# Performance work log

Measured on AMD Instinct MI355X. Metric: run time of the kernel, lower is better.

Reference implementation:

```python
import jax, jax.numpy as jnp
import numpy as np

D_IN = 1024
D_OUT = 1024
NUM_HEADS = 16
HEAD_DIM = D_OUT // NUM_HEADS


def setup_inputs() -> dict:
    key = jax.random.key(0)
    ks = jax.random.split(key, 6)
    s = 0.02
    return {
        "x": jax.random.normal(ks[0], (4, 2048, D_IN), dtype=jnp.float32),
        "W_q": jax.random.normal(ks[1], (D_IN, D_OUT), dtype=jnp.float32) * s,
        "W_k": jax.random.normal(ks[2], (D_IN, D_OUT), dtype=jnp.float32) * s,
        "W_v": jax.random.normal(ks[3], (D_IN, D_OUT), dtype=jnp.float32) * s,
        "W_o": jax.random.normal(ks[4], (D_OUT, D_OUT), dtype=jnp.float32) * s,
        "b_o": jax.random.normal(ks[5], (D_OUT,), dtype=jnp.float32) * s,
    }


def reference(x, W_q, W_k, W_v, W_o, b_o):
    b, n, _ = x.shape
    # project and split heads: [b, h, n, d]
    q = (x @ W_q).reshape(b, n, NUM_HEADS, HEAD_DIM).transpose(0, 2, 1, 3)
    k = (x @ W_k).reshape(b, n, NUM_HEADS, HEAD_DIM).transpose(0, 2, 1, 3)
    v = (x @ W_v).reshape(b, n, NUM_HEADS, HEAD_DIM).transpose(0, 2, 1, 3)
    scores = jnp.einsum("bhqd,bhkd->bhqk", q, k)
    causal = jnp.tril(jnp.ones((n, n), dtype=bool))  # True = keep
    scores = jnp.where(causal, scores, -jnp.inf)
    attn = jax.nn.softmax(scores / np.sqrt(HEAD_DIM).astype(np.float32), axis=-1)
    ctx = jnp.einsum("bhqk,bhkd->bhqd", attn, v)
    ctx = ctx.transpose(0, 2, 1, 3).reshape(b, n, D_OUT)
    return ctx @ W_o + b_o
```

## Files before the change

kernel.cpp:

```cpp
#include <hip/hip_runtime.h>
#include <hip/hip_bf16.h>

#define NHEADS 16
#define HDIM 64
#define SEQ 2048
#define BATCH 4
#define DMODEL 1024
#define MTOT (BATCH * SEQ)

typedef short v8s __attribute__((ext_vector_type(8)));
typedef short v4s __attribute__((ext_vector_type(4)));
typedef float v4f __attribute__((ext_vector_type(4)));
typedef float v16f __attribute__((ext_vector_type(16)));
typedef unsigned int v4u __attribute__((ext_vector_type(4)));
typedef unsigned short u16;
typedef unsigned int u32;

__device__ __forceinline__ u16 f2bf(float f) {
    union { float f; unsigned u; } v; v.f = f;
    unsigned r = v.u + 0x7FFFu + ((v.u >> 16) & 1u);
    return (u16)(r >> 16);
}

__device__ __forceinline__ void g2l16(const u16* g, short* l) {
    __builtin_amdgcn_global_load_lds(
        (const __attribute__((address_space(1))) u32*)g,
        (__attribute__((address_space(3))) u32*)l, 16, 0, 0);
}

__device__ __forceinline__ unsigned pk_bf16(float a, float b) {
    unsigned r;
    asm("v_cvt_pk_bf16_f32 %0, %1, %2" : "=v"(r) : "v"(a), "v"(b));
    return r;
}
__device__ __forceinline__ void pl32swap(unsigned& x, unsigned& y) {
    asm("v_permlane32_swap_b32 %0, %1" : "+v"(x), "+v"(y));
}
__device__ __forceinline__ v8s build_pa(float a0, float a1, float a2, float a3,
                                        float b0, float b1, float b2, float b3) {
    unsigned X  = pk_bf16(a0, a1);
    unsigned X2 = pk_bf16(a2, a3);
    unsigned Y  = pk_bf16(b0, b1);
    unsigned Y2 = pk_bf16(b2, b3);
    pl32swap(X, Y);
    pl32swap(X2, Y2);
    v4u w; w[0] = X; w[1] = X2; w[2] = Y; w[3] = Y2;
    return __builtin_bit_cast(v8s, w);
}

__global__ __launch_bounds__(256)
void xcvt(const float* __restrict__ x, u16* __restrict__ xb)
{
    size_t i = ((size_t)blockIdx.x * 256 + threadIdx.x) * 8;
    v4f a = *(const v4f*)&x[i];
    v4f b = *(const v4f*)&x[i + 4];
    v8s p;
#pragma unroll
    for (int e = 0; e < 4; ++e) p[e] = (short)f2bf(a[e]);
#pragma unroll
    for (int e = 0; e < 4; ++e) p[4 + e] = (short)f2bf(b[e]);
    *(v8s*)&xb[i] = p;
}

__device__ __forceinline__ void transpose_body(
    const float* __restrict__ src, u16* __restrict__ dst, int k0, int n0)
{
    __shared__ __align__(8) short Ts[64 * 68];
    const int t = threadIdx.x;
    const int n4 = (t & 15) * 4, kl = t >> 4;
#pragma unroll
    for (int it = 0; it < 4; ++it) {
        int k = kl + 16 * it;
        v4f v = *(const v4f*)&src[(size_t)(k0 + k) * DMODEL + n0 + n4];
        v4s p;
#pragma unroll
        for (int e = 0; e < 4; ++e) p[e] = (short)f2bf(v[e]);
        *(v4s*)&Ts[k * 68 + n4] = p;
    }
    __syncthreads();
    const int nl = t >> 4, k4 = (t & 15) * 4;
#pragma unroll
    for (int it = 0; it < 4; ++it) {
        int n = nl + 16 * it;
        v4s o;
#pragma unroll
        for (int e = 0; e < 4; ++e) o[e] = Ts[(k4 + e) * 68 + n];
        *(v4s*)&dst[(size_t)(n0 + n) * DMODEL + k0 + k4] = o;
    }
}

__global__ __launch_bounds__(256)
void transpose_w(const float* __restrict__ src, u16* __restrict__ dst)
{
    transpose_body(src, dst, blockIdx.x * 64, blockIdx.y * 64);
}

__global__ __launch_bounds__(256)
void transpose_w4(const float* __restrict__ s0, const float* __restrict__ s1,
                  const float* __restrict__ s2, const float* __restrict__ s3,
                  u16* __restrict__ dst)
{
    const int z = blockIdx.z;
    const float* src = (z == 0) ? s0 : (z == 1) ? s1 : (z == 2) ? s2 : s3;
    transpose_body(src, dst + (size_t)z * DMODEL * DMODEL,
                   blockIdx.x * 64, blockIdx.y * 64);
}

#define QSCALE (0.125f * 1.44269504088896f)

__device__ __forceinline__ void qkv_epilogue(
    v4f (&acc)[4][4], int which, int n0, int m0, int wn, int wm,
    int l15, int quad, u16* Qb, u16* Kb, u16* Vt)
{
    if (which == 2) {
#pragma unroll
        for (int i = 0; i < 4; ++i)
#pragma unroll
            for (int j = 0; j < 4; ++j) {
                int col = n0 + wn + j * 16 + l15;
                int h = col >> 6, d = col & 63;
                int m = m0 + wm + i * 16 + quad * 4;
                int b = m >> 11, n = m & (SEQ - 1);
                v4s pv;
#pragma unroll
                for (int r = 0; r < 4; ++r) pv[r] = (short)f2bf(acc[i][j][r]);
                *(v4s*)&Vt[((size_t)(b * NHEADS + h) * HDIM + d) * SEQ + n] = pv;
            }
    } else {
        u16* Ob = (which == 0) ? Qb : Kb;
        const float scale = (which == 0) ? QSCALE : 1.0f;
#pragma unroll
        for (int i = 0; i < 4; ++i)
#pragma unroll
            for (int j = 0; j < 4; ++j) {
                int col = n0 + wn + j * 16 + l15;
                int h = col >> 6, d = col & 63;
#pragma unroll
                for (int r = 0; r < 4; ++r) {
                    int m = m0 + wm + i * 16 + quad * 4 + r;
                    int b = m >> 11, n = m & (SEQ - 1);
                    Ob[((size_t)(b * NHEADS + h) * SEQ + n) * HDIM + d] =
                        f2bf(acc[i][j][r] * scale);
                }
            }
    }
}

__global__ __launch_bounds__(256, 2)
void qkv_fast(const u16* __restrict__ xb, const u16* __restrict__ Wt,
              u16* __restrict__ Qb, u16* __restrict__ Kb, u16* __restrict__ Vt)
{
    __shared__ __align__(16) short As[128 * 64];
    __shared__ __align__(16) short Bs[128 * 64];

    const int which = blockIdx.z;
    const u16* W = Wt + (size_t)which * DMODEL * DMODEL;

    const int n0 = blockIdx.x * 128;
    const int m0 = blockIdx.y * 128;
    const int t = threadIdx.x;
    const int lane = t & 63;
    const int l15 = lane & 15;
    const int quad = lane >> 4;
    const int wave = t >> 6;
    const int wm = (wave >> 1) * 64;
    const int wn = (wave & 1) * 64;
    const int srow = t >> 3;
    const int sc8 = (t & 7) * 8;

    v4f acc[4][4];
#pragma unroll
    for (int i = 0; i < 4; ++i)
#pragma unroll
        for (int j = 0; j < 4; ++j) acc[i][j] = {0.f, 0.f, 0.f, 0.f};

    for (int k0 = 0; k0 < DMODEL; k0 += 64) {
        __syncthreads();
#pragma unroll
        for (int c = 0; c < 4; ++c) {
            g2l16(&xb[(size_t)(m0 + c * 32 + srow) * DMODEL + k0 + sc8],
                  &As[(c * 32 + srow) * 64 + sc8]);
            g2l16(&W[(size_t)(n0 + c * 32 + srow) * DMODEL + k0 + sc8],
                  &Bs[(c * 32 + srow) * 64 + sc8]);
        }
        __syncthreads();

#pragma unroll
        for (int kh = 0; kh < 2; ++kh) {
            v8s af[4], bf[4];
#pragma unroll
            for (int i = 0; i < 4; ++i)
                af[i] = *(const v8s*)
                    &As[(wm + i * 16 + l15) * 64 + kh * 32 + quad * 8];
#pragma unroll
            for (int j = 0; j < 4; ++j)
                bf[j] = *(const v8s*)
                    &Bs[(wn + j * 16 + l15) * 64 + kh * 32 + quad * 8];
#pragma unroll
            for (int i = 0; i < 4; ++i)
#pragma unroll
                for (int j = 0; j < 4; ++j)
                    acc[i][j] = __builtin_amdgcn_mfma_f32_16x16x32_bf16(
                        af[i], bf[j], acc[i][j], 0, 0, 0);
        }
    }
    qkv_epilogue(acc, which, n0, m0, wn, wm, l15, quad, Qb, Kb, Vt);
}

__global__ __launch_bounds__(256, 2)
void qkv_slow(const float* __restrict__ x, const u16* __restrict__ Wt,
              u16* __restrict__ Qb, u16* __restrict__ Kb, u16* __restrict__ Vt)
{
    __shared__ __align__(16) short As[128 * 32];
    __shared__ __align__(16) short Bs[128 * 32];

    const int which = blockIdx.z;
    const u16* W = Wt + (size_t)which * DMODEL * DMODEL;

    const int n0 = blockIdx.x * 128;
    const int m0 = blockIdx.y * 128;
    const int t = threadIdx.x;
    const int lane = t & 63;
    const int l15 = lane & 15;
    const int quad = lane >> 4;
    const int wave = t >> 6;
    const int wm = (wave >> 1) * 64;
    const int wn = (wave & 1) * 64;
    const int srow = t >> 2;
    const int sc8 = (t & 3) * 8;

    v4f acc[4][4];
#pragma unroll
    for (int i = 0; i < 4; ++i)
#pragma unroll
        for (int j = 0; j < 4; ++j) acc[i][j] = {0.f, 0.f, 0.f, 0.f};

    for (int k0 = 0; k0 < DMODEL; k0 += 32) {
        __syncthreads();
        g2l16(&W[(size_t)(n0 + srow) * DMODEL + k0 + sc8], &Bs[srow * 32 + sc8]);
        g2l16(&W[(size_t)(n0 + 64 + srow) * DMODEL + k0 + sc8],
              &Bs[(64 + srow) * 32 + sc8]);
#pragma unroll
        for (int it = 0; it < 2; ++it) {
            int row = srow + 64 * it;
            const float* xp = &x[(size_t)(m0 + row) * DMODEL + k0 + sc8];
            v4f x0 = *(const v4f*)xp;
            v4f x1 = *(const v4f*)(xp + 4);
            v8s av;
#pragma unroll
            for (int e = 0; e < 4; ++e) av[e] = (short)f2bf(x0[e]);
#pragma unroll
            for (int e = 0; e < 4; ++e) av[4 + e] = (short)f2bf(x1[e]);
            *(v8s*)&As[row * 32 + sc8] = av;
        }
        __syncthreads();

        v8s af[4], bf[4];
#pragma unroll
        for (int i = 0; i < 4; ++i)
            af[i] = *(const v8s*)&As[(wm + i * 16 + l15) * 32 + quad * 8];
#pragma unroll
        for (int j = 0; j < 4; ++j)
            bf[j] = *(const v8s*)&Bs[(wn + j * 16 + l15) * 32 + quad * 8];
#pragma unroll
        for (int i = 0; i < 4; ++i)
#pragma unroll
            for (int j = 0; j < 4; ++j)
                acc[i][j] = __builtin_amdgcn_mfma_f32_16x16x32_bf16(
                    af[i], bf[j], acc[i][j], 0, 0, 0);
    }
    qkv_epilogue(acc, which, n0, m0, wn, wm, l15, quad, Qb, Kb, Vt);
}

#define KP 72

__global__ __launch_bounds__(256, 2)
void attn(const u16* __restrict__ Qb, const u16* __restrict__ Kb,
          const u16* __restrict__ Vt, u16* __restrict__ Cx)
{
    __shared__ __align__(16) short Ks[64 * KP];
    __shared__ __align__(16) short Vs[64 * KP];

    const int ell = blockIdx.x;
    const int xcd = ell & 7;
    const int rest = ell >> 3;
    const int p = rest & 7;
    const int bh = ((rest >> 3) << 3) | xcd;

    const int t = threadIdx.x;
    const int lane = t & 63;
    const int l31 = lane & 31;
    const int hi = lane >> 5;
    const int wave = t >> 6;
    const int koff = hi * 8;

    const u16* Qh = Qb + (size_t)bh * SEQ * HDIM;
    const u16* Kh = Kb + (size_t)bh * SEQ * HDIM;
    const u16* Vh = Vt + (size_t)bh * HDIM * SEQ;

    const int skey = t >> 2;
    const int sd = (t & 3) * 16;
    const int b = bh >> 4, h = bh & 15;

#pragma unroll 1
    for (int phase = 0; phase < 2; ++phase) {
        const int qt = phase ? p : (15 - p);
        const int q0w = qt * 128 + wave * 32;
        const int kmax = 2 * qt + 1;

        v8s qf[4];
#pragma unroll
        for (int dc = 0; dc < 4; ++dc)
            qf[dc] = *(const v8s*)
                &Qh[(size_t)(q0w + l31) * HDIM + dc * 16 + koff];

        v16f o0, o1;
#pragma unroll
        for (int r = 0; r < 16; ++r) { o0[r] = 0.f; o1[r] = 0.f; }
        float ls = 0.f;

        v8s pk0_, pk1_, pv0_, pv1_;
        {
            const u16* Kp = &Kh[(size_t)skey * HDIM + sd];
            pk0_ = *(const v8s*)Kp; pk1_ = *(const v8s*)(Kp + 8);
            const u16* Vp = &Vh[(size_t)skey * SEQ + sd];
            pv0_ = *(const v8s*)Vp; pv1_ = *(const v8s*)(Vp + 8);
        }

#pragma unroll 1
        for (int kb = 0; kb <= kmax; ++kb) {
            __syncthreads();
            *(v8s*)&Ks[skey * KP + sd] = pk0_;
            *(v8s*)&Ks[skey * KP + sd + 8] = pk1_;
            *(v8s*)&Vs[skey * KP + sd] = pv0_;
            *(v8s*)&Vs[skey * KP + sd + 8] = pv1_;
            __syncthreads();

            if (kb < kmax) {
                const u16* Kp = &Kh[(size_t)((kb + 1) * 64 + skey) * HDIM + sd];
                pk0_ = *(const v8s*)Kp; pk1_ = *(const v8s*)(Kp + 8);
                const u16* Vp = &Vh[(size_t)skey * SEQ + (kb + 1) * 64 + sd];
                pv0_ = *(const v8s*)Vp; pv1_ = *(const v8s*)(Vp + 8);
            }

            if (kb * 64 <= q0w + 31) {
                const bool diag = (kb * 64 + 63 > q0w);
                const int qrow = q0w + l31;

                v16f st0, st1;
#pragma unroll
                for (int r = 0; r < 16; ++r) { st0[r] = 0.f; st1[r] = 0.f; }
#pragma unroll
                for (int dc = 0; dc < 4; ++dc) {
                    v8s kf0 = *(const v8s*)&Ks[l31 * KP + dc * 16 + koff];
                    v8s kf1 = *(const v8s*)
                        &Ks[(32 + l31) * KP + dc * 16 + koff];
                    st0 = __builtin_amdgcn_mfma_f32_32x32x16_bf16(
                        kf0, qf[dc], st0, 0, 0, 0);
                    st1 = __builtin_amdgcn_mfma_f32_32x32x16_bf16(
                        kf1, qf[dc], st1, 0, 0, 0);
                }

                v16f pe0, pe1;
                if (!diag) {
#pragma unroll
                    for (int r = 0; r < 16; ++r) {
                        pe0[r] = exp2f(st0[r]);
                        pe1[r] = exp2f(st1[r]);
                    }
                } else {
#pragma unroll
                    for (int r = 0; r < 16; ++r) {
                        int kl = kb * 64 + (r & 3) + 8 * (r >> 2) + 4 * hi;
                        pe0[r] = (kl > qrow) ? 0.f : exp2f(st0[r]);
                        pe1[r] = (kl + 32 > qrow) ? 0.f : exp2f(st1[r]);
                    }
                }
#pragma unroll
                for (int r = 0; r < 16; ++r) ls += pe0[r] + pe1[r];

                v8s pa0 = build_pa(pe0[0], pe0[1], pe0[2], pe0[3],
                                   pe0[4], pe0[5], pe0[6], pe0[7]);
                v8s pa1 = build_pa(pe0[8], pe0[9], pe0[10], pe0[11],
                                   pe0[12], pe0[13], pe0[14], pe0[15]);
                v8s pa2 = build_pa(pe1[0], pe1[1], pe1[2], pe1[3],
                                   pe1[4], pe1[5], pe1[6], pe1[7]);
                v8s pa3 = build_pa(pe1[8], pe1[9], pe1[10], pe1[11],
                                   pe1[12], pe1[13], pe1[14], pe1[15]);

#pragma unroll
                for (int kc = 0; kc < 4; ++kc) {
                    v8s pav = (kc == 0) ? pa0 : (kc == 1) ? pa1
                              : (kc == 2) ? pa2 : pa3;
                    v8s vf0 = *(const v8s*)&Vs[l31 * KP + kc * 16 + koff];
                    v8s vf1 = *(const v8s*)
                        &Vs[(32 + l31) * KP + kc * 16 + koff];
                    o0 = __builtin_amdgcn_mfma_f32_32x32x16_bf16(
                        pav, vf0, o0, 0, 0, 0);
                    o1 = __builtin_amdgcn_mfma_f32_32x32x16_bf16(
                        pav, vf1, o1, 0, 0, 0);
                }
            }
        }

        ls += __shfl_xor(ls, 32, 64);
        float inv = 1.f / ls;
#pragma unroll
        for (int r = 0; r < 16; ++r) {
            int m = (r & 3) + 8 * (r >> 2) + 4 * hi;
            float im = __shfl(inv, m, 64);
            size_t idx = ((size_t)(b * SEQ + q0w + m)) * DMODEL
                         + h * HDIM + l31;
            Cx[idx] = f2bf(o0[r] * im);
            Cx[idx + 32] = f2bf(o1[r] * im);
        }
    }
}

__global__ __launch_bounds__(256, 2)
void out_gemm(const u16* __restrict__ Cx, const u16* __restrict__ WoT,
              const float* __restrict__ bo, float* __restrict__ Y)
{
    __shared__ __align__(16) short As[128 * 64];
    __shared__ __align__(16) short Bs[128 * 64];

    const int n0 = blockIdx.x * 128;
    const int m0 = blockIdx.y * 128;
    const int t = threadIdx.x;
    const int lane = t & 63;
    const int l15 = lane & 15;
    const int quad = lane >> 4;
    const int wave = t >> 6;
    const int wm = (wave >> 1) * 64;
    const int wn = (wave & 1) * 64;
    const int srow = t >> 3;
    const int sc8 = (t & 7) * 8;

    v4f acc[4][4];
#pragma unroll
    for (int i = 0; i < 4; ++i)
#pragma unroll
        for (int j = 0; j < 4; ++j) acc[i][j] = {0.f, 0.f, 0.f, 0.f};

    for (int k0 = 0; k0 < DMODEL; k0 += 64) {
        __syncthreads();
#pragma unroll
        for (int c = 0; c < 4; ++c) {
            g2l16(&Cx[(size_t)(m0 + c * 32 + srow) * DMODEL + k0 + sc8],
                  &As[(c * 32 + srow) * 64 + sc8]);
            g2l16(&WoT[(size_t)(n0 + c * 32 + srow) * DMODEL + k0 + sc8],
                  &Bs[(c * 32 + srow) * 64 + sc8]);
        }
        __syncthreads();

#pragma unroll
        for (int kh = 0; kh < 2; ++kh) {
            v8s af[4], bf[4];
#pragma unroll
            for (int i = 0; i < 4; ++i)
                af[i] = *(const v8s*)
                    &As[(wm + i * 16 + l15) * 64 + kh * 32 + quad * 8];
#pragma unroll
            for (int j = 0; j < 4; ++j)
                bf[j] = *(const v8s*)
                    &Bs[(wn + j * 16 + l15) * 64 + kh * 32 + quad * 8];
#pragma unroll
            for (int i = 0; i < 4; ++i)
#pragma unroll
                for (int j = 0; j < 4; ++j)
                    acc[i][j] = __builtin_amdgcn_mfma_f32_16x16x32_bf16(
                        af[i], bf[j], acc[i][j], 0, 0, 0);
        }
    }

#pragma unroll
    for (int i = 0; i < 4; ++i)
#pragma unroll
        for (int j = 0; j < 4; ++j) {
            int col = n0 + wn + j * 16 + l15;
            float bias = bo[col];
#pragma unroll
            for (int r = 0; r < 4; ++r) {
                int m = m0 + wm + i * 16 + quad * 4 + r;
                Y[(size_t)m * DMODEL + col] = acc[i][j][r] + bias;
            }
        }
}

extern "C" void kernel_launch(void* const* d_in, const int* in_sizes, int n_in,
                              void* d_out, int out_size, void* d_ws,
                              size_t ws_size, hipStream_t stream)
{
    const float* x  = (const float*)d_in[0];
    const float* Wq = (const float*)d_in[1];
    const float* Wk = (const float*)d_in[2];
    const float* Wv = (const float*)d_in[3];
    const float* Wo = (const float*)d_in[4];
    const float* bo = (const float*)d_in[5];
    float* Y = (float*)d_out;

    const size_t per = (size_t)BATCH * NHEADS * SEQ * HDIM;
    const size_t wsz = (size_t)DMODEL * DMODEL;
    u16* base = (u16*)d_ws;

    if (ws_size >= (size_t)72 * 1024 * 1024) {
        u16* xb  = base;
        u16* Cx  = base;
        u16* Wt4 = base + per;
        u16* Qb  = base + per + 4 * wsz;
        u16* Kb  = Qb + per;
        u16* Vt  = Kb + per;

        xcvt<<<MTOT * DMODEL / (256 * 8), 256, 0, stream>>>(x, xb);
        transpose_w4<<<dim3(16, 16, 4), 256, 0, stream>>>(Wq, Wk, Wv, Wo, Wt4);
        qkv_fast<<<dim3(DMODEL / 128, MTOT / 128, 3), 256, 0, stream>>>(
            xb, Wt4, Qb, Kb, Vt);
        attn<<<512, 256, 0, stream>>>(Qb, Kb, Vt, Cx);
        out_gemm<<<dim3(DMODEL / 128, MTOT / 128), 256, 0, stream>>>(
            Cx, Wt4 + 3 * wsz, bo, Y);
    } else {
        u16* Wt  = base;
        u16* Cx  = base;
        u16* Qb  = base + per;
        u16* WoT = base + per;
        u16* Kb  = base + 2 * per;
        u16* Vt  = base + 3 * per;

        transpose_w<<<dim3(16, 16), 256, 0, stream>>>(Wq, Wt);
        transpose_w<<<dim3(16, 16), 256, 0, stream>>>(Wk, Wt + wsz);
        transpose_w<<<dim3(16, 16), 256, 0, stream>>>(Wv, Wt + 2 * wsz);
        qkv_slow<<<dim3(DMODEL / 128, MTOT / 128, 3), 256, 0, stream>>>(
            x, Wt, Qb, Kb, Vt);
        attn<<<512, 256, 0, stream>>>(Qb, Kb, Vt, Cx);
        transpose_w<<<dim3(16, 16), 256, 0, stream>>>(Wo, WoT);
        out_gemm<<<dim3(DMODEL / 128, MTOT / 128), 256, 0, stream>>>(
            Cx, WoT, bo, Y);
    }
}
```

Before: 266.5 us.

## Replace QKV GEMM with 256x256 double-buffered pipelined kernel over fused QKV

Swaps the 128x128 single-buffered QKV projection kernel for a 512-thread kernel with 256x256 tiles that treats the three weight matrices as one concatenated N=3072 operand. The new kernel double-buffers LDS, overlaps global-to-LDS staging with MFMA work across four sub-phases, applies an XOR swizzle to LDS to avoid bank conflicts, raises wave priority around MFMA blocks, and remaps block ids for better L2 locality. The aim is more operand reuse and better load/compute overlap in the GEMM. In exchange it uses much more LDS (128 KB) and registers, which limits occupancy, and it depends on hand-tuned waitcnt/barrier ordering.

```diff
diff --git a/kernel.cpp b/kernel.cpp
--- a/kernel.cpp
+++ b/kernel.cpp
@@ -108,6 +108,162 @@
 
 #define QSCALE (0.125f * 1.44269504088896f)
 
+#define BAR() __builtin_amdgcn_s_barrier()
+#define LGKM0() do { asm volatile("s_waitcnt lgkmcnt(0)" ::: "memory"); \
+                     __builtin_amdgcn_sched_barrier(0); } while (0)
+
+#define STAGE_A(sbuf, stile, half, issue) \
+    g2l16(&xb[(size_t)(m0 + (half) * 128 + (issue) * 64 + srr) * DMODEL + \
+              (stile) * 64 + scol], \
+          &As[sbuf][(half) * 8192 + (issue) * 4096 + t * 8])
+#define STAGE_B(sbuf, stile, half, issue) \
+    g2l16(&Wt[(size_t)(n0g + (half) * 128 + (issue) * 64 + srr) * DMODEL + \
+              (stile) * 64 + scol], \
+          &Bs[sbuf][(half) * 8192 + (issue) * 4096 + t * 8])
+
+#define LDA_QUAD(bb, I0) \
+    _Pragma("unroll") \
+    for (int i = 0; i < 4; ++i) \
+        _Pragma("unroll") \
+        for (int kh = 0; kh < 2; ++kh) \
+            af[i][kh] = *(const v8s*)&As[bb][ \
+                (wm * 128 + ((I0) + i) * 16 + l15) * 64 + \
+                (((kh * 4 + quad) ^ (l15 & 7)) << 3)];
+
+#define LDB_PAIR(bb, J0) \
+    _Pragma("unroll") \
+    for (int j = 0; j < 2; ++j) \
+        _Pragma("unroll") \
+        for (int kh = 0; kh < 2; ++kh) \
+            bf[(J0) + j][kh] = *(const v8s*)&Bs[bb][ \
+                (wn * 64 + ((J0) + j) * 16 + l15) * 64 + \
+                (((kh * 4 + quad) ^ (l15 & 7)) << 3)];
+
+#define MFMA_QUAD(I0, J0) \
+    _Pragma("unroll") \
+    for (int i = 0; i < 4; ++i) \
+        _Pragma("unroll") \
+        for (int j = 0; j < 2; ++j) \
+            _Pragma("unroll") \
+            for (int kh = 0; kh < 2; ++kh) \
+                acc[(I0) + i][(J0) + j] = \
+                    __builtin_amdgcn_mfma_f32_16x16x32_bf16( \
+                        af[i][kh], bf[(J0) + j][kh], \
+                        acc[(I0) + i][(J0) + j], 0, 0, 0);
+
+__global__ __launch_bounds__(512, 2)
+void qkv256(const u16* __restrict__ xb, const u16* __restrict__ Wt,
+            u16* __restrict__ Qb, u16* __restrict__ Kb, u16* __restrict__ Vt)
+{
+    __shared__ __align__(16) short As[2][256 * 64];
+    __shared__ __align__(16) short Bs[2][256 * 64];
+
+    const int bid = blockIdx.x;
+    const int swz = (bid & 7) * 48 + (bid >> 3);
+    const int bx = swz % 12, by = swz / 12;
+    const int n0g = bx * 256;
+    const int m0 = by * 256;
+
+    const int t = threadIdx.x;
+    const int lane = t & 63;
+    const int l15 = lane & 15;
+    const int quad = lane >> 4;
+    const int wave = t >> 6;
+    const int wm = wave >> 2;
+    const int wn = wave & 3;
+
+    const int srr = t >> 3;
+    const int scol = (((t & 7) ^ (srr & 7)) << 3);
+
+    v4f acc[8][4];
+#pragma unroll
+    for (int i = 0; i < 8; ++i)
+#pragma unroll
+        for (int j = 0; j < 4; ++j) acc[i][j] = {0.f, 0.f, 0.f, 0.f};
+
+    STAGE_A(0, 0, 0, 0); STAGE_A(0, 0, 0, 1);
+    STAGE_A(0, 0, 1, 0); STAGE_A(0, 0, 1, 1);
+    STAGE_B(0, 0, 0, 0); STAGE_B(0, 0, 0, 1);
+    STAGE_B(0, 0, 1, 0); STAGE_B(0, 0, 1, 1);
+    STAGE_B(1, 1, 0, 0); STAGE_B(1, 1, 0, 1);
+    STAGE_B(1, 1, 1, 0); STAGE_B(1, 1, 1, 1);
+    asm volatile("s_waitcnt vmcnt(4)" ::: "memory");
+    BAR();
+
+#pragma unroll 1
+    for (int tt = 0; tt < 16; ++tt) {
+        const int cb = tt & 1;
+        v8s af[4][2];
+        v8s bf[4][2];
+
+        LDA_QUAD(cb, 0);
+        LDB_PAIR(cb, 0);
+        if (tt < 15) { STAGE_A(cb ^ 1, tt + 1, 0, 0);
+                       STAGE_A(cb ^ 1, tt + 1, 0, 1); }
+        BAR();
+        LGKM0();
+        __builtin_amdgcn_s_setprio(1);
+        MFMA_QUAD(0, 0);
+        __builtin_amdgcn_s_setprio(0);
+        BAR();
+
+        LDB_PAIR(cb, 2);
+        if (tt < 15) { STAGE_A(cb ^ 1, tt + 1, 1, 0);
+                       STAGE_A(cb ^ 1, tt + 1, 1, 1); }
+        BAR();
+        LGKM0();
+        __builtin_amdgcn_s_setprio(1);
+        MFMA_QUAD(0, 2);
+        __builtin_amdgcn_s_setprio(0);
+        BAR();
+
+        LDA_QUAD(cb, 4);
+        if (tt < 14) { STAGE_B(cb, tt + 2, 0, 0);
+                       STAGE_B(cb, tt + 2, 0, 1); }
+        BAR();
+        LGKM0();
+        __builtin_amdgcn_s_setprio(1);
+        MFMA_QUAD(4, 2);
+        __builtin_amdgcn_s_setprio(0);
+        BAR();
+
+        if (tt < 14) { STAGE_B(cb, tt + 2, 1, 0);
+                       STAGE_B(cb, tt + 2, 1, 1); }
+        BAR();
+        __builtin_amdgcn_s_setprio(1);
+        MFMA_QUAD(4, 0);
+        __builtin_amdgcn_s_setprio(0);
+        if (tt < 14)      asm volatile("s_waitcnt vmcnt(4)" ::: "memory");
+        else if (tt == 14) asm volatile("s_waitcnt vmcnt(0)" ::: "memory");
+        BAR();
+    }
+
+#pragma unroll
+    for (int i = 0; i < 8; ++i)
+#pragma unroll
+        for (int j = 0; j < 4; ++j) {
+            int col = n0g + wn * 64 + j * 16 + l15;
+            int which = col >> 10;
+            int w = col & 1023;
+            int h = w >> 6, d = w & 63;
+            int mbase = m0 + wm * 128 + i * 16 + quad * 4;
+            int bb = mbase >> 11, n = mbase & (SEQ - 1);
+            if (which == 2) {
+                v4s pv;
+#pragma unroll
+                for (int r = 0; r < 4; ++r) pv[r] = (short)f2bf(acc[i][j][r]);
+                *(v4s*)&Vt[((size_t)(bb * NHEADS + h) * HDIM + d) * SEQ + n] = pv;
+            } else {
+                u16* Ob = which ? Kb : Qb;
+                const float scale = which ? 1.0f : QSCALE;
+#pragma unroll
+                for (int r = 0; r < 4; ++r)
+                    Ob[((size_t)(bb * NHEADS + h) * SEQ + n + r) * HDIM + d] =
+                        f2bf(acc[i][j][r] * scale);
+            }
+        }
+}
+
 __device__ __forceinline__ void qkv_epilogue(
     v4f (&acc)[4][4], int which, int n0, int m0, int wn, int wm,
     int l15, int quad, u16* Qb, u16* Kb, u16* Vt)
@@ -144,67 +300,6 @@
                 }
             }
     }
-}
-
-__global__ __launch_bounds__(256, 2)
-void qkv_fast(const u16* __restrict__ xb, const u16* __restrict__ Wt,
-              u16* __restrict__ Qb, u16* __restrict__ Kb, u16* __restrict__ Vt)
-{
-    __shared__ __align__(16) short As[128 * 64];
-    __shared__ __align__(16) short Bs[128 * 64];
-
-    const int which = blockIdx.z;
-    const u16* W = Wt + (size_t)which * DMODEL * DMODEL;
-
-    const int n0 = blockIdx.x * 128;
-    const int m0 = blockIdx.y * 128;
-    const int t = threadIdx.x;
-    const int lane = t & 63;
-    const int l15 = lane & 15;
-    const int quad = lane >> 4;
-    const int wave = t >> 6;
-    const int wm = (wave >> 1) * 64;
-    const int wn = (wave & 1) * 64;
-    const int srow = t >> 3;
-    const int sc8 = (t & 7) * 8;
-
-    v4f acc[4][4];
-#pragma unroll
-    for (int i = 0; i < 4; ++i)
-#pragma unroll
-        for (int j = 0; j < 4; ++j) acc[i][j] = {0.f, 0.f, 0.f, 0.f};
-
-    for (int k0 = 0; k0 < DMODEL; k0 += 64) {
-        __syncthreads();
-#pragma unroll
-        for (int c = 0; c < 4; ++c) {
-            g2l16(&xb[(size_t)(m0 + c * 32 + srow) * DMODEL + k0 + sc8],
-                  &As[(c * 32 + srow) * 64 + sc8]);
-            g2l16(&W[(size_t)(n0 + c * 32 + srow) * DMODEL + k0 + sc8],
-                  &Bs[(c * 32 + srow) * 64 + sc8]);
-        }
-        __syncthreads();
-
-#pragma unroll
-        for (int kh = 0; kh < 2; ++kh) {
-            v8s af[4], bf[4];
-#pragma unroll
-            for (int i = 0; i < 4; ++i)
-                af[i] = *(const v8s*)
-                    &As[(wm + i * 16 + l15) * 64 + kh * 32 + quad * 8];
-#pragma unroll
-            for (int j = 0; j < 4; ++j)
-                bf[j] = *(const v8s*)
-                    &Bs[(wn + j * 16 + l15) * 64 + kh * 32 + quad * 8];
-#pragma unroll
-            for (int i = 0; i < 4; ++i)
-#pragma unroll
-                for (int j = 0; j < 4; ++j)
-                    acc[i][j] = __builtin_amdgcn_mfma_f32_16x16x32_bf16(
-                        af[i], bf[j], acc[i][j], 0, 0, 0);
-        }
-    }
-    qkv_epilogue(acc, which, n0, m0, wn, wm, l15, quad, Qb, Kb, Vt);
 }
 
 __global__ __launch_bounds__(256, 2)
@@ -513,8 +608,7 @@
 
         xcvt<<<MTOT * DMODEL / (256 * 8), 256, 0, stream>>>(x, xb);
         transpose_w4<<<dim3(16, 16, 4), 256, 0, stream>>>(Wq, Wk, Wv, Wo, Wt4);
-        qkv_fast<<<dim3(DMODEL / 128, MTOT / 128, 3), 256, 0, stream>>>(
-            xb, Wt4, Qb, Kb, Vt);
+        qkv256<<<384, 512, 0, stream>>>(xb, Wt4, Qb, Kb, Vt);
         attn<<<512, 256, 0, stream>>>(Qb, Kb, Vt, Cx);
         out_gemm<<<dim3(DMODEL / 128, MTOT / 128), 256, 0, stream>>>(
             Cx, Wt4 + 3 * wsz, bo, Y);
```

New measurement: 258.0 us. 3.2% less time.

## Widen attention K/V tile to 128 keys with XOR-swizzled LDS layout

Applied to the files above, without the earlier changes.

The attention kernel now stages 128 keys of K and V per iteration instead of 64, which halves the number of barrier-separated load/compute iterations. Padded LDS rows are replaced by XOR-swizzled 16-byte slots to avoid bank conflicts. Each staging pass issues more global loads, using more registers and twice the LDS per block. That may reduce occupancy, and some of each tile is skipped on the causal boundary.

```diff
diff --git a/kernel.cpp b/kernel.cpp
--- a/kernel.cpp
+++ b/kernel.cpp
@@ -272,14 +272,14 @@
     qkv_epilogue(acc, which, n0, m0, wn, wm, l15, quad, Qb, Kb, Vt);
 }
 
-#define KP 72
+#define VXOR(d) ((((d) & 7) << 1) | (((d) >> 3) & 1))
 
 __global__ __launch_bounds__(256, 2)
 void attn(const u16* __restrict__ Qb, const u16* __restrict__ Kb,
           const u16* __restrict__ Vt, u16* __restrict__ Cx)
 {
-    __shared__ __align__(16) short Ks[64 * KP];
-    __shared__ __align__(16) short Vs[64 * KP];
+    __shared__ __align__(16) short Ks[128 * 64];
+    __shared__ __align__(16) short Vs[64 * 128];
 
     const int ell = blockIdx.x;
     const int xcd = ell & 7;
@@ -298,15 +298,16 @@
     const u16* Kh = Kb + (size_t)bh * SEQ * HDIM;
     const u16* Vh = Vt + (size_t)bh * HDIM * SEQ;
 
-    const int skey = t >> 2;
-    const int sd = (t & 3) * 16;
+    const int krow = t >> 3;
+    const int kslot = t & 7;
+    const int vrow = t >> 4;
+    const int vslot = t & 15;
     const int b = bh >> 4, h = bh & 15;
 
 #pragma unroll 1
     for (int phase = 0; phase < 2; ++phase) {
         const int qt = phase ? p : (15 - p);
         const int q0w = qt * 128 + wave * 32;
-        const int kmax = 2 * qt + 1;
 
         v8s qf[4];
 #pragma unroll
@@ -319,32 +320,48 @@
         for (int r = 0; r < 16; ++r) { o0[r] = 0.f; o1[r] = 0.f; }
         float ls = 0.f;
 
-        v8s pk0_, pk1_, pv0_, pv1_;
-        {
-            const u16* Kp = &Kh[(size_t)skey * HDIM + sd];
-            pk0_ = *(const v8s*)Kp; pk1_ = *(const v8s*)(Kp + 8);
-            const u16* Vp = &Vh[(size_t)skey * SEQ + sd];
-            pv0_ = *(const v8s*)Vp; pv1_ = *(const v8s*)(Vp + 8);
-        }
+        v8s pk[4], pv[4];
+#pragma unroll
+        for (int it = 0; it < 4; ++it)
+            pk[it] = *(const v8s*)
+                &Kh[(size_t)(it * 32 + krow) * HDIM + kslot * 8];
+#pragma unroll
+        for (int it = 0; it < 4; ++it)
+            pv[it] = *(const v8s*)
+                &Vh[(size_t)(it * 16 + vrow) * SEQ + vslot * 8];
 
 #pragma unroll 1
-        for (int kb = 0; kb <= kmax; ++kb) {
+        for (int kb = 0; kb <= qt; ++kb) {
             __syncthreads();
-            *(v8s*)&Ks[skey * KP + sd] = pk0_;
-            *(v8s*)&Ks[skey * KP + sd + 8] = pk1_;
-            *(v8s*)&Vs[skey * KP + sd] = pv0_;
-            *(v8s*)&Vs[skey * KP + sd + 8] = pv1_;
+#pragma unroll
+            for (int it = 0; it < 4; ++it) {
+                int row = it * 32 + krow;
+                *(v8s*)&Ks[row * 64 + ((kslot ^ (row & 7)) << 3)] = pk[it];
+            }
+#pragma unroll
+            for (int it = 0; it < 4; ++it) {
+                int d = it * 16 + vrow;
+                *(v8s*)&Vs[d * 128 + ((vslot ^ VXOR(d)) << 3)] = pv[it];
+            }
             __syncthreads();
 
-            if (kb < kmax) {
-                const u16* Kp = &Kh[(size_t)((kb + 1) * 64 + skey) * HDIM + sd];
-                pk0_ = *(const v8s*)Kp; pk1_ = *(const v8s*)(Kp + 8);
-                const u16* Vp = &Vh[(size_t)skey * SEQ + (kb + 1) * 64 + sd];
-                pv0_ = *(const v8s*)Vp; pv1_ = *(const v8s*)(Vp + 8);
-            }
-
-            if (kb * 64 <= q0w + 31) {
-                const bool diag = (kb * 64 + 63 > q0w);
+            if (kb < qt) {
+                const int kn = (kb + 1) * 128;
+#pragma unroll
+                for (int it = 0; it < 4; ++it)
+                    pk[it] = *(const v8s*)
+                        &Kh[(size_t)(kn + it * 32 + krow) * HDIM + kslot * 8];
+#pragma unroll
+                for (int it = 0; it < 4; ++it)
+                    pv[it] = *(const v8s*)
+                        &Vh[(size_t)(it * 16 + vrow) * SEQ + kn + vslot * 8];
+            }
+
+#pragma unroll
+            for (int k2 = 0; k2 < 2; ++k2) {
+                const int kbase = kb * 128 + k2 * 64;
+                if (kbase > q0w + 31) continue;
+                const bool diag = (kbase + 63 > q0w);
                 const int qrow = q0w + l31;
 
                 v16f st0, st1;
@@ -352,9 +369,13 @@
                 for (int r = 0; r < 16; ++r) { st0[r] = 0.f; st1[r] = 0.f; }
 #pragma unroll
                 for (int dc = 0; dc < 4; ++dc) {
-                    v8s kf0 = *(const v8s*)&Ks[l31 * KP + dc * 16 + koff];
+                    const int ds = dc * 2 + hi;
+                    const int r0 = k2 * 64 + l31;
+                    const int r1 = k2 * 64 + 32 + l31;
+                    v8s kf0 = *(const v8s*)
+                        &Ks[r0 * 64 + ((ds ^ (r0 & 7)) << 3)];
                     v8s kf1 = *(const v8s*)
-                        &Ks[(32 + l31) * KP + dc * 16 + koff];
+                        &Ks[r1 * 64 + ((ds ^ (r1 & 7)) << 3)];
                     st0 = __builtin_amdgcn_mfma_f32_32x32x16_bf16(
                         kf0, qf[dc], st0, 0, 0, 0);
                     st1 = __builtin_amdgcn_mfma_f32_32x32x16_bf16(
@@ -371,7 +392,7 @@
                 } else {
 #pragma unroll
                     for (int r = 0; r < 16; ++r) {
-                        int kl = kb * 64 + (r & 3) + 8 * (r >> 2) + 4 * hi;
+                        int kl = kbase + (r & 3) + 8 * (r >> 2) + 4 * hi;
                         pe0[r] = (kl > qrow) ? 0.f : exp2f(st0[r]);
                         pe1[r] = (kl + 32 > qrow) ? 0.f : exp2f(st1[r]);
                     }
@@ -392,9 +413,12 @@
                 for (int kc = 0; kc < 4; ++kc) {
                     v8s pav = (kc == 0) ? pa0 : (kc == 1) ? pa1
                               : (kc == 2) ? pa2 : pa3;
-                    v8s vf0 = *(const v8s*)&Vs[l31 * KP + kc * 16 + koff];
+                    const int ks = k2 * 8 + kc * 2 + hi;
+                    const int d0 = l31, d1 = 32 + l31;
+                    v8s vf0 = *(const v8s*)
+                        &Vs[d0 * 128 + ((ks ^ VXOR(d0)) << 3)];
                     v8s vf1 = *(const v8s*)
-                        &Vs[(32 + l31) * KP + kc * 16 + koff];
+                        &Vs[d1 * 128 + ((ks ^ VXOR(d1)) << 3)];
                     o0 = __builtin_amdgcn_mfma_f32_32x32x16_bf16(
                         pav, vf0, o0, 0, 0, 0);
                     o1 = __builtin_amdgcn_mfma_f32_32x32x16_bf16(
```

New measurement: 261.0 us. 1.02x faster.
